# Performance work log

Measured on AMD Instinct MI355X. Metric: run time of the kernel, lower is better.

The kernel has to match this reference:

```python
import jax, jax.numpy as jnp
import numpy as np


def setup_inputs() -> dict:
    key = jax.random.key(0)
    k1, k2 = jax.random.split(key)
    N, Cin, H, W = 32, 4096, 28, 28
    Cout = 4  # number of CAM classes (hard-coded /4 in the module)
    x = jax.random.normal(k1, (N, Cin, H, W), dtype=jnp.float32)
    fc_weights = jax.random.normal(k2, (Cout, Cin, 1, 1), dtype=jnp.float32) * 0.02
    gama = jnp.float32(0.7)
    return {"x": x, "fc_weights": fc_weights, "gama": gama}


def reference(x, fc_weights, gama):
    # cams = relu(conv2d(x, fc_weights)) with 1x1 kernel -> [N, Cout, H, W]
    w = fc_weights[:, :, 0, 0]  # [Cout, Cin]
    cams = jax.nn.relu(jnp.einsum('nchw,oc->nohw', x, w))
    # Per-channel spatial max over (H, W): [N, Cout, 1, 1]
    cam_max = jnp.max(cams, axis=(2, 3), keepdims=True)
    thr = cam_max * gama
    # Drop above-threshold activations, sum over channels (the C-loop), /4
    dropped = jnp.where(cams > thr, jnp.zeros((), cams.dtype), cams)
    mean_drop_cam = jnp.sum(dropped, axis=1, keepdims=True) / 4.0  # [N,1,H,W]
    # Final returned value: x modulated by the dropped-CAM spatial map
    return x * mean_drop_cam
```

## Files before the change

### kernel.cpp

```cpp
#include <hip/hip_runtime.h>

#define HW     784
#define HW4    196
#define CIN    4096
#define COUT   4
#define NIMG   32
#define CCHUNK 128
#define NCHUNK (CIN / CCHUNK)
#define F4_PER_IMG (CIN * HW4)
#define K3_SUB (CCHUNK * HW4 / 256)

typedef float f4raw __attribute__((ext_vector_type(4)));

__device__ __forceinline__ float4 f4zero() { return make_float4(0.f, 0.f, 0.f, 0.f); }

template <bool ATOMIC>
__global__ __launch_bounds__(256) void k1_cams(const float4* __restrict__ x4,
                                               const float*  __restrict__ w,
                                               float*        __restrict__ outbuf) {
    const int n  = blockIdx.x;
    const int cc = blockIdx.y;
    const int t  = threadIdx.x;

    __shared__ float4 wlds[CCHUNK];
    if (t < CCHUNK) {
        const int c = cc * CCHUNK + t;
        wlds[t] = make_float4(w[0 * CIN + c], w[1 * CIN + c],
                              w[2 * CIN + c], w[3 * CIN + c]);
    }
    __syncthreads();
    if (t >= HW4) return;

    const float4* xp = x4 + ((size_t)n * CIN + (size_t)cc * CCHUNK) * HW4 + t;

    float4 a0 = f4zero(), a1 = f4zero(), a2 = f4zero(), a3 = f4zero();
    #pragma unroll 8
    for (int c = 0; c < CCHUNK; ++c) {
        float4 xv = xp[(size_t)c * HW4];
        float4 wv = wlds[c];
        a0.x += xv.x * wv.x; a0.y += xv.y * wv.x; a0.z += xv.z * wv.x; a0.w += xv.w * wv.x;
        a1.x += xv.x * wv.y; a1.y += xv.y * wv.y; a1.z += xv.z * wv.y; a1.w += xv.w * wv.y;
        a2.x += xv.x * wv.z; a2.y += xv.y * wv.z; a2.z += xv.z * wv.z; a2.w += xv.w * wv.z;
        a3.x += xv.x * wv.w; a3.y += xv.y * wv.w; a3.z += xv.z * wv.w; a3.w += xv.w * wv.w;
    }

    if constexpr (ATOMIC) {
        float* cp = outbuf + (size_t)n * COUT * HW + 4 * t;
        atomicAdd(&cp[0 * HW + 0], a0.x); atomicAdd(&cp[0 * HW + 1], a0.y);
        atomicAdd(&cp[0 * HW + 2], a0.z); atomicAdd(&cp[0 * HW + 3], a0.w);
        atomicAdd(&cp[1 * HW + 0], a1.x); atomicAdd(&cp[1 * HW + 1], a1.y);
        atomicAdd(&cp[1 * HW + 2], a1.z); atomicAdd(&cp[1 * HW + 3], a1.w);
        atomicAdd(&cp[2 * HW + 0], a2.x); atomicAdd(&cp[2 * HW + 1], a2.y);
        atomicAdd(&cp[2 * HW + 2], a2.z); atomicAdd(&cp[2 * HW + 3], a2.w);
        atomicAdd(&cp[3 * HW + 0], a3.x); atomicAdd(&cp[3 * HW + 1], a3.y);
        atomicAdd(&cp[3 * HW + 2], a3.z); atomicAdd(&cp[3 * HW + 3], a3.w);
    } else {
        float4* pp = (float4*)outbuf +
                     (((size_t)n * NCHUNK + cc) * COUT) * HW4 + t;
        pp[0 * HW4] = a0;
        pp[1 * HW4] = a1;
        pp[2 * HW4] = a2;
        pp[3 * HW4] = a3;
    }
}

__global__ __launch_bounds__(256) void k2_scale(const float4* __restrict__ part,
                                                int P,
                                                const float* __restrict__ gama_p,
                                                float* __restrict__ s) {
    const int n = blockIdx.x;
    const int t = threadIdx.x;
    const float gama = gama_p[0];

    float4 c0 = f4zero(), c1 = f4zero(), c2 = f4zero(), c3 = f4zero();
    if (t < HW4) {
        for (int p = 0; p < P; ++p) {
            const float4* pp = part + ((size_t)(n * P + p) * COUT) * HW4 + t;
            float4 v0 = pp[0 * HW4], v1 = pp[1 * HW4], v2 = pp[2 * HW4], v3 = pp[3 * HW4];
            c0.x += v0.x; c0.y += v0.y; c0.z += v0.z; c0.w += v0.w;
            c1.x += v1.x; c1.y += v1.y; c1.z += v1.z; c1.w += v1.w;
            c2.x += v2.x; c2.y += v2.y; c2.z += v2.z; c2.w += v2.w;
            c3.x += v3.x; c3.y += v3.y; c3.z += v3.z; c3.w += v3.w;
        }
    }
    c0.x = fmaxf(c0.x, 0.f); c0.y = fmaxf(c0.y, 0.f); c0.z = fmaxf(c0.z, 0.f); c0.w = fmaxf(c0.w, 0.f);
    c1.x = fmaxf(c1.x, 0.f); c1.y = fmaxf(c1.y, 0.f); c1.z = fmaxf(c1.z, 0.f); c1.w = fmaxf(c1.w, 0.f);
    c2.x = fmaxf(c2.x, 0.f); c2.y = fmaxf(c2.y, 0.f); c2.z = fmaxf(c2.z, 0.f); c2.w = fmaxf(c2.w, 0.f);
    c3.x = fmaxf(c3.x, 0.f); c3.y = fmaxf(c3.y, 0.f); c3.z = fmaxf(c3.z, 0.f); c3.w = fmaxf(c3.w, 0.f);

    __shared__ float red[COUT][256];
    red[0][t] = (t < HW4) ? fmaxf(fmaxf(c0.x, c0.y), fmaxf(c0.z, c0.w)) : 0.f;
    red[1][t] = (t < HW4) ? fmaxf(fmaxf(c1.x, c1.y), fmaxf(c1.z, c1.w)) : 0.f;
    red[2][t] = (t < HW4) ? fmaxf(fmaxf(c2.x, c2.y), fmaxf(c2.z, c2.w)) : 0.f;
    red[3][t] = (t < HW4) ? fmaxf(fmaxf(c3.x, c3.y), fmaxf(c3.z, c3.w)) : 0.f;
    __syncthreads();
    for (int str = 128; str > 0; str >>= 1) {
        if (t < str) {
            #pragma unroll
            for (int o = 0; o < COUT; ++o)
                red[o][t] = fmaxf(red[o][t], red[o][t + str]);
        }
        __syncthreads();
    }
    const float t0 = red[0][0] * gama;
    const float t1 = red[1][0] * gama;
    const float t2 = red[2][0] * gama;
    const float t3 = red[3][0] * gama;

    if (t < HW4) {
        float4 sv;
        sv.x = (((c0.x > t0) ? 0.f : c0.x) + ((c1.x > t1) ? 0.f : c1.x) +
                ((c2.x > t2) ? 0.f : c2.x) + ((c3.x > t3) ? 0.f : c3.x)) * 0.25f;
        sv.y = (((c0.y > t0) ? 0.f : c0.y) + ((c1.y > t1) ? 0.f : c1.y) +
                ((c2.y > t2) ? 0.f : c2.y) + ((c3.y > t3) ? 0.f : c3.y)) * 0.25f;
        sv.z = (((c0.z > t0) ? 0.f : c0.z) + ((c1.z > t1) ? 0.f : c1.z) +
                ((c2.z > t2) ? 0.f : c2.z) + ((c3.z > t3) ? 0.f : c3.z)) * 0.25f;
        sv.w = (((c0.w > t0) ? 0.f : c0.w) + ((c1.w > t1) ? 0.f : c1.w) +
                ((c2.w > t2) ? 0.f : c2.w) + ((c3.w > t3) ? 0.f : c3.w)) * 0.25f;
        ((float4*)(s + (size_t)n * HW))[t] = sv;
    }
}

__global__ __launch_bounds__(256) void k3_mul(const f4raw* __restrict__ x4,
                                              const float* __restrict__ s,
                                              f4raw* __restrict__ out4) {
    const int bid   = blockIdx.x;
    const int ccRev = bid / (NIMG * K3_SUB);
    const int rem   = bid % (NIMG * K3_SUB);
    const int n     = rem / K3_SUB;
    const int sub   = rem % K3_SUB;
    const int cc    = NCHUNK - 1 - ccRev;

    const int f4InImg = cc * (CCHUNK * HW4) + sub * 256 + threadIdx.x;
    const int hw4     = f4InImg % HW4;
    const size_t idx  = (size_t)n * F4_PER_IMG + f4InImg;

    f4raw xv = __builtin_nontemporal_load(&x4[idx]);
    const f4raw* s4 = (const f4raw*)(s + (size_t)n * HW);
    f4raw sv = s4[hw4];
    f4raw ov = xv * sv;
    __builtin_nontemporal_store(ov, &out4[idx]);
}

extern "C" void kernel_launch(void* const* d_in, const int* in_sizes, int n_in,
                              void* d_out, int out_size, void* d_ws, size_t ws_size,
                              hipStream_t stream) {
    const float* x    = (const float*)d_in[0];
    const float* w    = (const float*)d_in[1];
    const float* gama = (const float*)d_in[2];
    float* out = (float*)d_out;

    const size_t part_floats = (size_t)NIMG * NCHUNK * COUT * HW;
    const size_t s_floats    = (size_t)NIMG * HW;
    const bool use_partials  = ws_size >= (part_floats + s_floats) * sizeof(float);

    if (use_partials) {
        float* part = (float*)d_ws;
        float* s    = part + part_floats;
        k1_cams<false><<<dim3(NIMG, NCHUNK), 256, 0, stream>>>(
            (const float4*)x, w, part);
        k2_scale<<<NIMG, 256, 0, stream>>>((const float4*)part, NCHUNK, gama, s);
        k3_mul<<<NCHUNK * NIMG * K3_SUB, 256, 0, stream>>>(
            (const f4raw*)x, s, (f4raw*)out);
    } else {
        float* cams_raw = (float*)d_ws;
        float* s        = cams_raw + (size_t)NIMG * COUT * HW;
        (void)hipMemsetAsync(cams_raw, 0, (size_t)NIMG * COUT * HW * sizeof(float), stream);
        k1_cams<true><<<dim3(NIMG, NCHUNK), 256, 0, stream>>>(
            (const float4*)x, w, cams_raw);
        k2_scale<<<NIMG, 256, 0, stream>>>((const float4*)cams_raw, 1, gama, s);
        k3_mul<<<NCHUNK * NIMG * K3_SUB, 256, 0, stream>>>(
            (const f4raw*)x, s, (f4raw*)out);
    }
}
```

Measured before the change: 730.0 us.

## Process the batch in image groups so the multiply pass re-reads x from cache

The three-kernel pipeline (partial CAM reduction, threshold/scale, elementwise multiply) now runs once per group of 8 images instead of once over the whole batch of 32. Each group's slice of x is about 100MB, small enough that it may still sit in the large last-level cache when the multiply kernel reads it again. This is meant to cut the second full HBM read of x. The multiply kernel's indexing becomes linear instead of reverse-chunk ordered. The cost is four times as many launches, and each reduction launch has only 256 blocks, which may lower memory parallelism in the first kernel.

```diff
diff --git a/kernel.cpp b/kernel.cpp
--- a/kernel.cpp
+++ b/kernel.cpp
@@ -8,7 +8,8 @@
 #define CCHUNK 128
 #define NCHUNK (CIN / CCHUNK)
 #define F4_PER_IMG (CIN * HW4)
-#define K3_SUB (CCHUNK * HW4 / 256)
+#define GROUPS 4
+#define IMG_G  (NIMG / GROUPS)
 
 typedef float f4raw __attribute__((ext_vector_type(4)));
 
@@ -17,8 +18,9 @@
 template <bool ATOMIC>
 __global__ __launch_bounds__(256) void k1_cams(const float4* __restrict__ x4,
                                                const float*  __restrict__ w,
-                                               float*        __restrict__ outbuf) {
-    const int n  = blockIdx.x;
+                                               float*        __restrict__ outbuf,
+                                               int n0) {
+    const int n  = n0 + blockIdx.x;
     const int cc = blockIdx.y;
     const int t  = threadIdx.x;
 
@@ -67,8 +69,9 @@
 __global__ __launch_bounds__(256) void k2_scale(const float4* __restrict__ part,
                                                 int P,
                                                 const float* __restrict__ gama_p,
-                                                float* __restrict__ s) {
-    const int n = blockIdx.x;
+                                                float* __restrict__ s,
+                                                int n0) {
+    const int n = n0 + blockIdx.x;
     const int t = threadIdx.x;
     const float gama = gama_p[0];
 
@@ -123,17 +126,13 @@
 
 __global__ __launch_bounds__(256) void k3_mul(const f4raw* __restrict__ x4,
                                               const float* __restrict__ s,
-                                              f4raw* __restrict__ out4) {
-    const int bid   = blockIdx.x;
-    const int ccRev = bid / (NIMG * K3_SUB);
-    const int rem   = bid % (NIMG * K3_SUB);
-    const int n     = rem / K3_SUB;
-    const int sub   = rem % K3_SUB;
-    const int cc    = NCHUNK - 1 - ccRev;
-
-    const int f4InImg = cc * (CCHUNK * HW4) + sub * 256 + threadIdx.x;
-    const int hw4     = f4InImg % HW4;
-    const size_t idx  = (size_t)n * F4_PER_IMG + f4InImg;
+                                              f4raw* __restrict__ out4,
+                                              int n0) {
+    const size_t g   = (size_t)blockIdx.x * 256 + threadIdx.x;
+    const int n_loc  = (int)(g / F4_PER_IMG);
+    const int hw4    = (int)(g % HW4);
+    const int n      = n0 + n_loc;
+    const size_t idx = (size_t)n0 * F4_PER_IMG + g;
 
     f4raw xv = __builtin_nontemporal_load(&x4[idx]);
     const f4raw* s4 = (const f4raw*)(s + (size_t)n * HW);
@@ -157,19 +156,24 @@
     if (use_partials) {
         float* part = (float*)d_ws;
         float* s    = part + part_floats;
-        k1_cams<false><<<dim3(NIMG, NCHUNK), 256, 0, stream>>>(
-            (const float4*)x, w, part);
-        k2_scale<<<NIMG, 256, 0, stream>>>((const float4*)part, NCHUNK, gama, s);
-        k3_mul<<<NCHUNK * NIMG * K3_SUB, 256, 0, stream>>>(
-            (const f4raw*)x, s, (f4raw*)out);
+        for (int grp = 0; grp < GROUPS; ++grp) {
+            const int n0 = grp * IMG_G;
+            k1_cams<false><<<dim3(IMG_G, NCHUNK), 256, 0, stream>>>(
+                (const float4*)x, w, part, n0);
+            k2_scale<<<IMG_G, 256, 0, stream>>>(
+                (const float4*)part, NCHUNK, gama, s, n0);
+            k3_mul<<<IMG_G * (F4_PER_IMG / 256), 256, 0, stream>>>(
+                (const f4raw*)x, s, (f4raw*)out, n0);
+        }
     } else {
         float* cams_raw = (float*)d_ws;
         float* s        = cams_raw + (size_t)NIMG * COUT * HW;
         (void)hipMemsetAsync(cams_raw, 0, (size_t)NIMG * COUT * HW * sizeof(float), stream);
         k1_cams<true><<<dim3(NIMG, NCHUNK), 256, 0, stream>>>(
-            (const float4*)x, w, cams_raw);
-        k2_scale<<<NIMG, 256, 0, stream>>>((const float4*)cams_raw, 1, gama, s);
-        k3_mul<<<NCHUNK * NIMG * K3_SUB, 256, 0, stream>>>(
-            (const f4raw*)x, s, (f4raw*)out);
+            (const float4*)x, w, cams_raw, 0);
+        k2_scale<<<NIMG, 256, 0, stream>>>(
+            (const float4*)cams_raw, 1, gama, s, 0);
+        k3_mul<<<NIMG * (F4_PER_IMG / 256), 256, 0, stream>>>(
+            (const f4raw*)x, s, (f4raw*)out, 0);
     }
 }
```

New measurement: 755.9 us. 3.5% more time.
